# Optimization experiments

Hardware: AMD Instinct MI355X
Metric: run time of the kernel (lower is better)

Reference implementation:

```python
import jax, jax.numpy as jnp
import numpy as np

B, T = 32, 50
CONCEPT_NUM = 500
C = CONCEPT_NUM + 1          # self.concept_num = concept_num + 1
H, E = 32, 32                # hidden_dim, embedding_dim
BN_SCALE = 1.0 / np.sqrt(1.0 + 1e-5)  # eval-mode BatchNorm1d, default running stats


def _mlp(x, w1, b1, w2, b2):
    # MLP: relu(fc1) -> (dropout off in eval) -> relu(fc2) -> BatchNorm1d(eval)
    x = jax.nn.relu(x @ w1.T + b1)
    x = jax.nn.relu(x @ w2.T + b2)
    return x * BN_SCALE


def _gru(x, h, w_ih, w_hh, b_ih, b_hh):
    # torch.nn.GRUCell semantics; gate order r, z, n
    gx = x @ w_ih.T + b_ih
    gh = h @ w_hh.T + b_hh
    hd = h.shape[-1]
    r = jax.nn.sigmoid(gx[..., :hd] + gh[..., :hd])
    z = jax.nn.sigmoid(gx[..., hd:2 * hd] + gh[..., hd:2 * hd])
    n = jnp.tanh(gx[..., 2 * hd:] + r * gh[..., 2 * hd:])
    return (1.0 - z) * n + z * h


def setup_inputs() -> dict:
    key = jax.random.key(0)
    ks = jax.random.split(key, 32)
    HE = H + E
    def lin(k, out_d, in_d):
        return jax.random.normal(k, (out_d, in_d), jnp.float32) * (1.0 / np.sqrt(in_d))
    inp = {
        'features': jax.random.randint(ks[0], (B, T), 0, 2 * C, jnp.int64),
        'questions': jax.random.randint(ks[1], (B, T), 0, C, jnp.int64),
        'graph': jax.random.uniform(ks[2], (C, C), jnp.float32),
        'emb_x': jax.random.normal(ks[3], (2 * C, E), jnp.float32),
        'emb_c': jax.random.normal(ks[4], (C, E), jnp.float32),
        # f_self: MLP(H+E -> H -> H)
        'self_w1': lin(ks[5], H, HE), 'self_b1': jnp.full((H,), 0.1, jnp.float32),
        'self_w2': lin(ks[6], H, H),  'self_b2': jnp.full((H,), 0.1, jnp.float32),
        # f_neighbor_list[0]: MLP(2*(H+E) -> H -> H)
        'n0_w1': lin(ks[7], H, 2 * HE), 'n0_b1': jnp.full((H,), 0.1, jnp.float32),
        'n0_w2': lin(ks[8], H, H),      'n0_b2': jnp.full((H,), 0.1, jnp.float32),
        # f_neighbor_list[1]
        'n1_w1': lin(ks[9], H, 2 * HE),  'n1_b1': jnp.full((H,), 0.1, jnp.float32),
        'n1_w2': lin(ks[10], H, H),      'n1_b2': jnp.full((H,), 0.1, jnp.float32),
        # EraseAddGate
        'ea_w': jax.random.uniform(ks[11], (C,), jnp.float32, -1.0, 1.0) / np.sqrt(C),
        'ea_ew': lin(ks[12], H, H), 'ea_eb': jnp.zeros((H,), jnp.float32),
        'ea_aw': lin(ks[13], H, H), 'ea_ab': jnp.zeros((H,), jnp.float32),
        # GRUCell
        'gru_w_ih': lin(ks[14], 3 * H, H), 'gru_w_hh': lin(ks[15], 3 * H, H),
        'gru_b_ih': jnp.zeros((3 * H,), jnp.float32), 'gru_b_hh': jnp.zeros((3 * H,), jnp.float32),
        # predict
        'pred_w': lin(ks[16], 1, H), 'pred_b': jnp.zeros((1,), jnp.float32),
    }
    return inp


def reference(features, questions, graph, emb_x, emb_c,
              self_w1, self_b1, self_w2, self_b2,
              n0_w1, n0_b1, n0_w2, n0_b2,
              n1_w1, n1_b1, n1_w2, n1_b2,
              ea_w, ea_ew, ea_eb, ea_aw, ea_ab,
              gru_w_ih, gru_w_hh, gru_b_ih, gru_b_hh,
              pred_w, pred_b):
    b_ar = jnp.arange(B)

    def step(ht, inp):
        xt, qt = inp  # [B], [B]
        # _aggregate: response embedding via one_hot(xt) @ emb_x == gather
        res_emb = emb_x[xt]                                          # [B, E]
        ce = jnp.broadcast_to(emb_c[None], (B, C, E))                # [B, C, E]
        ce = ce.at[b_ar, qt].set(res_emb)
        tmp_ht = jnp.concatenate([ht, ce], axis=-1)                  # [B, C, H+E]
        # _agg_neighbors (Dense graph, 2 edge types)
        self_ht = tmp_ht[b_ar, qt]                                   # [B, H+E]
        self_feat = _mlp(self_ht, self_w1, self_b1, self_w2, self_b2)
        neigh_ht = jnp.concatenate(
            [jnp.broadcast_to(self_ht[:, None], tmp_ht.shape), tmp_ht], axis=-1)  # [B, C, 2(H+E)]
        adj = graph[qt][..., None]                                   # [B, C, 1]
        radj = graph[:, qt].T[..., None]                             # [B, C, 1]
        neigh = adj * _mlp(neigh_ht, n0_w1, n0_b1, n0_w2, n0_b2) \
              + radj * _mlp(neigh_ht, n1_w1, n1_b1, n1_w2, n1_b2)    # [B, C, H]
        m = neigh.at[b_ar, qt].set(self_feat)
        # EraseAddGate
        eg = jax.nn.sigmoid(m @ ea_ew.T + ea_eb)
        af = jnp.tanh(m @ ea_aw.T + ea_ab)
        w = ea_w[None, :, None]
        m = m - w * eg * m + w * af
        # GRUCell over every (student, concept)
        h_next = _gru(m.reshape(-1, H), ht.reshape(-1, H),
                      gru_w_ih, gru_w_hh, gru_b_ih, gru_b_hh).reshape(B, C, H)
        yt = jax.nn.sigmoid((h_next @ pred_w.T + pred_b)[..., 0])    # [B, C]
        return h_next, yt

    ht0 = jnp.zeros((B, C, H), dtype=graph.dtype)
    _, yts = jax.lax.scan(step, ht0, (features.T, questions.T))      # [T, B, C]
    # _get_next_pred: prediction for question at t+1 from state after step t
    yts = jnp.moveaxis(yts[:-1], 0, 1)                               # [B, T-1, C]
    q_next = questions[:, 1:]                                        # [B, T-1]
    pred = jnp.take_along_axis(yts, q_next[..., None], axis=-1)[..., 0]
    return pred                                                      # [B, T-1]
```

## Files before the change

### kernel.cpp

```cpp
#include <hip/hip_runtime.h>
#include <math.h>

#define BB 32
#define TT 50
#define CC 501
#define NNODES (BB*CC)
#define GPB 32
#define NTHREADS (GPB*32)
#define NBLK (NNODES/GPB)
#define BN_SCALEF 0.9999950000374996f

#define HT_SZ   (NNODES*32)
#define P_SZ    (CC*32)
#define GT_SZ   (CC*CC)
#define PERB_BUF (BB*96)

__device__ __forceinline__ float dot4(float4 a, float4 b){
    return a.x*b.x + a.y*b.y + a.z*b.z + a.w*b.w;
}
__device__ __forceinline__ float sigm(float x){ return 1.f/(1.f+__expf(-x)); }
__device__ __forceinline__ float tanhfast(float x){ return 1.f - 2.f/(__expf(2.f*x)+1.f); }

__global__ void init0_kernel(const float* __restrict__ graph,
                             float* __restrict__ graphT,
                             float* __restrict__ ht) {
    int i = blockIdx.x*blockDim.x + threadIdx.x;
    if (i < HT_SZ) ht[i] = 0.f;
    if (i < GT_SZ) {
        int r = i / CC, c2 = i % CC;
        graphT[i] = graph[c2*CC + r];
    }
}

__global__ void pk_kernel(const float* __restrict__ n0_w1, const float* __restrict__ n1_w1,
                          const float* __restrict__ emb_c,
                          float* __restrict__ P0, float* __restrict__ P1) {
    int c = blockIdx.x;
    int which = threadIdx.x >> 5, j = threadIdx.x & 31;
    float ec = emb_c[c*32 + j];
    const float* W = which ? n1_w1 : n0_w1;
    float acc = 0.f;
    #pragma unroll
    for (int k = 0; k < 32; k++)
        acc += W[j*128 + 96 + k] * __shfl(ec, k, 32);
    (which ? P1 : P0)[c*32 + j] = acc;
}

__global__ void perb0_kernel(const int* __restrict__ features, const float* __restrict__ emb_x,
                             const float* __restrict__ n0_w1, const float* __restrict__ n0_b1,
                             const float* __restrict__ n1_w1, const float* __restrict__ n1_b1,
                             const float* __restrict__ self_w1, const float* __restrict__ self_b1,
                             const float* __restrict__ self_w2, const float* __restrict__ self_b2,
                             float* __restrict__ perb) {
    int b = threadIdx.x >> 5, j = threadIdx.x & 31;
    int xt = features[b*TT + 0];
    float eq = emb_x[xt*32 + j];
    float a0 = n0_b1[j], a1 = n1_b1[j], s = self_b1[j];
    #pragma unroll
    for (int k = 0; k < 32; k++) {
        float ek = __shfl(eq, k, 32);
        a0 += n0_w1[j*128 + 32 + k] * ek;
        a1 += n1_w1[j*128 + 32 + k] * ek;
        s  += self_w1[j*64 + 32 + k] * ek;
    }
    float l1 = fmaxf(s, 0.f);
    float s2 = self_b2[j];
    #pragma unroll
    for (int k = 0; k < 32; k++) s2 += self_w2[j*32 + k] * __shfl(l1, k, 32);
    perb[b*96 + j]      = a0;
    perb[b*96 + 32 + j] = a1;
    perb[b*96 + 64 + j] = fmaxf(s2, 0.f) * BN_SCALEF;
}

__global__ __launch_bounds__(NTHREADS) void step_kernel(
    int t,
    const int* __restrict__ features, const int* __restrict__ questions,
    const float* __restrict__ graph,  const float* __restrict__ emb_x,
    const float* __restrict__ self_w1, const float* __restrict__ self_b1,
    const float* __restrict__ self_w2, const float* __restrict__ self_b2,
    const float* __restrict__ n0_w1, const float* __restrict__ n0_b1,
    const float* __restrict__ n0_w2, const float* __restrict__ n0_b2,
    const float* __restrict__ n1_w1, const float* __restrict__ n1_b1,
    const float* __restrict__ n1_w2, const float* __restrict__ n1_b2,
    const float* __restrict__ ea_w,  const float* __restrict__ ea_ew,
    const float* __restrict__ ea_eb, const float* __restrict__ ea_aw,
    const float* __restrict__ ea_ab,
    const float* __restrict__ gru_w_ih, const float* __restrict__ gru_w_hh,
    const float* __restrict__ gru_b_ih, const float* __restrict__ gru_b_hh,
    const float* __restrict__ pred_w,   const float* __restrict__ pred_b,
    float* __restrict__ ht,
    const float* __restrict__ P0, const float* __restrict__ P1,
    const float* __restrict__ graphT,
    float* __restrict__ perb, float* __restrict__ out)
{
    __shared__ float Wq[12288];
    __shared__ float bufH[GPB][36];
    __shared__ float bufA[GPB][36];
    __shared__ float bufB[GPB][36];

    int tid = threadIdx.x;
    for (int idx = tid; idx < 12288; idx += NTHREADS) {
        float v;
        if (idx < 6144) {
            int region = idx >> 10;
            int r = idx & 1023;
            int j = (r >> 2) & 31;
            int k = ((r >> 7) << 2) | (r & 3);
            switch (region) {
                case 0:  v = n0_w1[j*128 + 64 + k]; break;
                case 1:  v = n1_w1[j*128 + 64 + k]; break;
                case 2:  v = n0_w2[j*32 + k]; break;
                case 3:  v = n1_w2[j*32 + k]; break;
                case 4:  v = ea_ew[j*32 + k]; break;
                default: v = ea_aw[j*32 + k]; break;
            }
            Wq[idx] = v;
        } else {
            int r = idx - 6144;
            int which = r / 3072;
            int r2 = r % 3072;
            int row = (r2 >> 2) % 96;
            int k = ((r2 / 384) << 2) | (r2 & 3);
            Wq[idx] = which ? gru_w_hh[row*32 + k] : gru_w_ih[row*32 + k];
        }
    }

    int g = tid >> 5, j = tid & 31;
    int node = blockIdx.x * GPB + g;
    int b = node / CC, c = node % CC;
    int qt = questions[b*TT + t];
    float adj  = graph [qt*CC + c];
    float radj = graphT[qt*CC + c];
    float h_j = ht[node*32 + j];
    bufH[g][j] = h_j;
    __syncthreads();

    const float* pb = perb + (t & 1) * PERB_BUF + b*96;

    float acc0 = pb[j]      + P0[c*32 + j];
    float acc1 = pb[32 + j] + P1[c*32 + j];
    {
        const float4* xh = (const float4*)bufH[g];
        #pragma unroll
        for (int kc = 0; kc < 8; kc++) {
            float4 x  = xh[kc];
            float4 w0 = *(const float4*)&Wq[       kc*128 + j*4];
            float4 w1 = *(const float4*)&Wq[1024 + kc*128 + j*4];
            acc0 += dot4(w0, x);
            acc1 += dot4(w1, x);
        }
    }
    bufA[g][j] = fmaxf(acc0, 0.f);
    bufB[g][j] = fmaxf(acc1, 0.f);

    float a0 = n0_b2[j], a1 = n1_b2[j];
    {
        const float4* xa = (const float4*)bufA[g];
        const float4* xb = (const float4*)bufB[g];
        #pragma unroll
        for (int kc = 0; kc < 8; kc++) {
            float4 va = xa[kc], vb = xb[kc];
            float4 w0 = *(const float4*)&Wq[2048 + kc*128 + j*4];
            float4 w1 = *(const float4*)&Wq[3072 + kc*128 + j*4];
            a0 += dot4(w0, va);
            a1 += dot4(w1, vb);
        }
    }
    float f0 = fmaxf(a0, 0.f) * BN_SCALEF;
    float f1 = fmaxf(a1, 0.f) * BN_SCALEF;
    float m = adj*f0 + radj*f1;
    if (c == qt) m = pb[64 + j];
    bufA[g][j] = m;

    float e = ea_eb[j], aa = ea_ab[j];
    {
        const float4* xm = (const float4*)bufA[g];
        #pragma unroll
        for (int kc = 0; kc < 8; kc++) {
            float4 vm = xm[kc];
            float4 we = *(const float4*)&Wq[4096 + kc*128 + j*4];
            float4 wa = *(const float4*)&Wq[5120 + kc*128 + j*4];
            e  += dot4(we, vm);
            aa += dot4(wa, vm);
        }
    }
    float eg = sigm(e);
    float af = tanhfast(aa);
    float wc = ea_w[c];
    float mm = m - wc*eg*m + wc*af;
    bufB[g][j] = mm;

    float g0 = gru_b_ih[j], g1 = gru_b_ih[32+j], g2 = gru_b_ih[64+j];
    float hh0 = gru_b_hh[j], hh1 = gru_b_hh[32+j], hh2 = gru_b_hh[64+j];
    {
        const float4* xm = (const float4*)bufB[g];
        const float4* xh = (const float4*)bufH[g];
        #pragma unroll
        for (int kc = 0; kc < 8; kc++) {
            float4 vm = xm[kc], vh = xh[kc];
            const float* wi = &Wq[6144 + kc*384];
            const float* wh = &Wq[9216 + kc*384];
            float4 wi0 = *(const float4*)&wi[j*4];
            float4 wi1 = *(const float4*)&wi[(32+j)*4];
            float4 wi2 = *(const float4*)&wi[(64+j)*4];
            float4 wh0 = *(const float4*)&wh[j*4];
            float4 wh1 = *(const float4*)&wh[(32+j)*4];
            float4 wh2 = *(const float4*)&wh[(64+j)*4];
            g0  += dot4(wi0, vm);  g1  += dot4(wi1, vm);  g2  += dot4(wi2, vm);
            hh0 += dot4(wh0, vh);  hh1 += dot4(wh1, vh);  hh2 += dot4(wh2, vh);
        }
    }
    float r = sigm(g0 + hh0);
    float z = sigm(g1 + hh1);
    float n = tanhfast(g2 + r*hh2);
    float hn = (1.f - z)*n + z*h_j;
    ht[node*32 + j] = hn;

    int qn = questions[b*TT + t + 1];
    if (c == qn) {
        float v = hn * pred_w[j];
        #pragma unroll
        for (int off = 16; off; off >>= 1) v += __shfl_down(v, off, 32);
        if (j == 0) out[b*(TT-1) + t] = sigm(v + pred_b[0]);

        if (t < TT - 2) {
            int xt1 = features[b*TT + t + 1];
            float eq = emb_x[xt1*32 + j];
            float accA0 = n0_b1[j], accA1 = n1_b1[j], accS = self_b1[j];
            #pragma unroll
            for (int k = 0; k < 32; k++) {
                float hk = __shfl(hn, k, 32);
                float ek = __shfl(eq, k, 32);
                accA0 += n0_w1[j*128 + k]*hk + n0_w1[j*128 + 32 + k]*ek;
                accA1 += n1_w1[j*128 + k]*hk + n1_w1[j*128 + 32 + k]*ek;
                accS  += self_w1[j*64 + k]*hk + self_w1[j*64 + 32 + k]*ek;
            }
            float l1 = fmaxf(accS, 0.f);
            float s2 = self_b2[j];
            #pragma unroll
            for (int k = 0; k < 32; k++) s2 += self_w2[j*32 + k] * __shfl(l1, k, 32);
            float* pn = perb + ((t+1) & 1) * PERB_BUF + b*96;
            pn[j]      = accA0;
            pn[32 + j] = accA1;
            pn[64 + j] = fmaxf(s2, 0.f) * BN_SCALEF;
        }
    }
}

extern "C" void kernel_launch(void* const* d_in, const int* in_sizes, int n_in,
                              void* d_out, int out_size, void* d_ws, size_t ws_size,
                              hipStream_t stream) {
    const int*   features = (const int*)  d_in[0];
    const int*   questions= (const int*)  d_in[1];
    const float* graph    = (const float*)d_in[2];
    const float* emb_x    = (const float*)d_in[3];
    const float* emb_c    = (const float*)d_in[4];
    const float* self_w1  = (const float*)d_in[5];
    const float* self_b1  = (const float*)d_in[6];
    const float* self_w2  = (const float*)d_in[7];
    const float* self_b2  = (const float*)d_in[8];
    const float* n0_w1    = (const float*)d_in[9];
    const float* n0_b1    = (const float*)d_in[10];
    const float* n0_w2    = (const float*)d_in[11];
    const float* n0_b2    = (const float*)d_in[12];
    const float* n1_w1    = (const float*)d_in[13];
    const float* n1_b1    = (const float*)d_in[14];
    const float* n1_w2    = (const float*)d_in[15];
    const float* n1_b2    = (const float*)d_in[16];
    const float* ea_w     = (const float*)d_in[17];
    const float* ea_ew    = (const float*)d_in[18];
    const float* ea_eb    = (const float*)d_in[19];
    const float* ea_aw    = (const float*)d_in[20];
    const float* ea_ab    = (const float*)d_in[21];
    const float* gru_w_ih = (const float*)d_in[22];
    const float* gru_w_hh = (const float*)d_in[23];
    const float* gru_b_ih = (const float*)d_in[24];
    const float* gru_b_hh = (const float*)d_in[25];
    const float* pred_w   = (const float*)d_in[26];
    const float* pred_b   = (const float*)d_in[27];
    float* out = (float*)d_out;

    float* ws     = (float*)d_ws;
    float* ht     = ws;
    float* P0     = ht + HT_SZ;
    float* P1     = P0 + P_SZ;
    float* graphT = P1 + P_SZ;
    float* perb   = graphT + GT_SZ;

    init0_kernel<<<(HT_SZ + 255)/256, 256, 0, stream>>>(graph, graphT, ht);
    pk_kernel<<<CC, 64, 0, stream>>>(n0_w1, n1_w1, emb_c, P0, P1);
    perb0_kernel<<<1, NTHREADS, 0, stream>>>(features, emb_x,
        n0_w1, n0_b1, n1_w1, n1_b1, self_w1, self_b1, self_w2, self_b2, perb);

    for (int t = 0; t < TT - 1; t++) {
        step_kernel<<<NBLK, NTHREADS, 0, stream>>>(
            t, features, questions, graph, emb_x,
            self_w1, self_b1, self_w2, self_b2,
            n0_w1, n0_b1, n0_w2, n0_b2,
            n1_w1, n1_b1, n1_w2, n1_b2,
            ea_w, ea_ew, ea_eb, ea_aw, ea_ab,
            gru_w_ih, gru_w_hh, gru_b_ih, gru_b_hh,
            pred_w, pred_b,
            ht, P0, P1, graphT, perb, out);
    }
}
```

Before: 1.017 ms.

## Process multiple nodes per thread to reuse shared-memory weight loads

Each 64-lane wave now handles 8 nodes, with every thread accumulating 4 nodes at once, so each float4 weight read from shared memory serves several nodes. Blocks shrink to 512 threads covering 64 nodes, which cuts the per-block weight-staging overhead relative to useful work and lowers the shared-memory weight traffic per FLOP. The cost is more registers per thread, which may reduce occupancy, and fewer, larger blocks.

New measurement: 1.128 ms. 1.11x slower.

```diff
diff --git a/kernel.cpp b/kernel.cpp
--- a/kernel.cpp
+++ b/kernel.cpp
@@ -5,10 +5,14 @@
 #define TT 50
 #define CC 501
 #define NNODES (BB*CC)
-#define GPB 32
-#define NTHREADS (GPB*32)
-#define NBLK (NNODES/GPB)
 #define BN_SCALEF 0.9999950000374996f
+
+#define V 4
+#define NPW 8
+#define WPB 8
+#define NTH 512
+#define NPB (NPW*WPB)
+#define NBLK ((NNODES + NPB - 1)/NPB)
 
 #define HT_SZ   (NNODES*32)
 #define P_SZ    (CC*32)
@@ -72,7 +76,7 @@
     perb[b*96 + 64 + j] = fmaxf(s2, 0.f) * BN_SCALEF;
 }
 
-__global__ __launch_bounds__(NTHREADS) void step_kernel(
+__global__ __launch_bounds__(NTH) void step_kernel(
     int t,
     const int* __restrict__ features, const int* __restrict__ questions,
     const float* __restrict__ graph,  const float* __restrict__ emb_x,
@@ -94,12 +98,10 @@
     float* __restrict__ perb, float* __restrict__ out)
 {
     __shared__ float Wq[12288];
-    __shared__ float bufH[GPB][36];
-    __shared__ float bufA[GPB][36];
-    __shared__ float bufB[GPB][36];
+    __shared__ float xb[WPB][3][NPW][32];
 
     int tid = threadIdx.x;
-    for (int idx = tid; idx < 12288; idx += NTHREADS) {
+    for (int idx = tid; idx < 12288; idx += NTH) {
         float v;
         if (idx < 6144) {
             int region = idx >> 10;
@@ -125,124 +127,186 @@
         }
     }
 
-    int g = tid >> 5, j = tid & 31;
-    int node = blockIdx.x * GPB + g;
-    int b = node / CC, c = node % CC;
-    int qt = questions[b*TT + t];
-    float adj  = graph [qt*CC + c];
-    float radj = graphT[qt*CC + c];
-    float h_j = ht[node*32 + j];
-    bufH[g][j] = h_j;
+    int l   = tid & 63;
+    int w   = tid >> 6;
+    int j   = l & 31, sub = l >> 5;
+    int nodebase = blockIdx.x*NPB + w*NPW;
+    bool act = nodebase < NNODES;
+
+    int nodev[V], bv[V], cv[V], qtv[V], pbo[V];
+    float hj[V], adjv[V], radjv[V];
+    if (act) {
+        #pragma unroll
+        for (int v = 0; v < V; v++) {
+            int node = nodebase + 2*v + sub;
+            nodev[v] = node;
+            int b = node / CC;
+            int c = node - b*CC;
+            bv[v] = b; cv[v] = c;
+            int qt = questions[b*TT + t];
+            qtv[v] = qt;
+            adjv[v]  = graph [qt*CC + c];
+            radjv[v] = graphT[qt*CC + c];
+            pbo[v] = (t & 1)*PERB_BUF + b*96;
+            float h = ht[node*32 + j];
+            hj[v] = h;
+            xb[w][0][2*v+sub][j] = h;
+        }
+    }
     __syncthreads();
-
-    const float* pb = perb + (t & 1) * PERB_BUF + b*96;
-
-    float acc0 = pb[j]      + P0[c*32 + j];
-    float acc1 = pb[32 + j] + P1[c*32 + j];
+    if (!act) return;
+
+    float acc0[V], acc1[V];
+    #pragma unroll
+    for (int v = 0; v < V; v++) {
+        acc0[v] = perb[pbo[v] + j]      + P0[cv[v]*32 + j];
+        acc1[v] = perb[pbo[v] + 32 + j] + P1[cv[v]*32 + j];
+    }
+    #pragma unroll
+    for (int kc = 0; kc < 8; kc++) {
+        float4 w0 = *(const float4*)&Wq[       kc*128 + j*4];
+        float4 w1 = *(const float4*)&Wq[1024 + kc*128 + j*4];
+        #pragma unroll
+        for (int v = 0; v < V; v++) {
+            float4 x = *(const float4*)&xb[w][0][2*v+sub][kc*4];
+            acc0[v] += dot4(w0, x);
+            acc1[v] += dot4(w1, x);
+        }
+    }
+    #pragma unroll
+    for (int v = 0; v < V; v++) {
+        xb[w][1][2*v+sub][j] = fmaxf(acc0[v], 0.f);
+        xb[w][2][2*v+sub][j] = fmaxf(acc1[v], 0.f);
+    }
+
+    float a0[V], a1[V];
     {
-        const float4* xh = (const float4*)bufH[g];
-        #pragma unroll
-        for (int kc = 0; kc < 8; kc++) {
-            float4 x  = xh[kc];
-            float4 w0 = *(const float4*)&Wq[       kc*128 + j*4];
-            float4 w1 = *(const float4*)&Wq[1024 + kc*128 + j*4];
-            acc0 += dot4(w0, x);
-            acc1 += dot4(w1, x);
-        }
-    }
-    bufA[g][j] = fmaxf(acc0, 0.f);
-    bufB[g][j] = fmaxf(acc1, 0.f);
-
-    float a0 = n0_b2[j], a1 = n1_b2[j];
+        float b0 = n0_b2[j], b1 = n1_b2[j];
+        #pragma unroll
+        for (int v = 0; v < V; v++) { a0[v] = b0; a1[v] = b1; }
+    }
+    #pragma unroll
+    for (int kc = 0; kc < 8; kc++) {
+        float4 w0 = *(const float4*)&Wq[2048 + kc*128 + j*4];
+        float4 w1 = *(const float4*)&Wq[3072 + kc*128 + j*4];
+        #pragma unroll
+        for (int v = 0; v < V; v++) {
+            float4 va = *(const float4*)&xb[w][1][2*v+sub][kc*4];
+            float4 vb = *(const float4*)&xb[w][2][2*v+sub][kc*4];
+            a0[v] += dot4(w0, va);
+            a1[v] += dot4(w1, vb);
+        }
+    }
+    float mval[V];
+    #pragma unroll
+    for (int v = 0; v < V; v++) {
+        float f0 = fmaxf(a0[v], 0.f) * BN_SCALEF;
+        float f1 = fmaxf(a1[v], 0.f) * BN_SCALEF;
+        float m = adjv[v]*f0 + radjv[v]*f1;
+        if (cv[v] == qtv[v]) m = perb[pbo[v] + 64 + j];
+        mval[v] = m;
+    }
+    #pragma unroll
+    for (int v = 0; v < V; v++) xb[w][1][2*v+sub][j] = mval[v];
+
+    float e[V], aa[V];
     {
-        const float4* xa = (const float4*)bufA[g];
-        const float4* xb = (const float4*)bufB[g];
-        #pragma unroll
-        for (int kc = 0; kc < 8; kc++) {
-            float4 va = xa[kc], vb = xb[kc];
-            float4 w0 = *(const float4*)&Wq[2048 + kc*128 + j*4];
-            float4 w1 = *(const float4*)&Wq[3072 + kc*128 + j*4];
-            a0 += dot4(w0, va);
-            a1 += dot4(w1, vb);
-        }
-    }
-    float f0 = fmaxf(a0, 0.f) * BN_SCALEF;
-    float f1 = fmaxf(a1, 0.f) * BN_SCALEF;
-    float m = adj*f0 + radj*f1;
-    if (c == qt) m = pb[64 + j];
-    bufA[g][j] = m;
-
-    float e = ea_eb[j], aa = ea_ab[j];
+        float be = ea_eb[j], ba = ea_ab[j];
+        #pragma unroll
+        for (int v = 0; v < V; v++) { e[v] = be; aa[v] = ba; }
+    }
+    #pragma unroll
+    for (int kc = 0; kc < 8; kc++) {
+        float4 we = *(const float4*)&Wq[4096 + kc*128 + j*4];
+        float4 wa = *(const float4*)&Wq[5120 + kc*128 + j*4];
+        #pragma unroll
+        for (int v = 0; v < V; v++) {
+            float4 vm = *(const float4*)&xb[w][1][2*v+sub][kc*4];
+            e[v]  += dot4(we, vm);
+            aa[v] += dot4(wa, vm);
+        }
+    }
+    #pragma unroll
+    for (int v = 0; v < V; v++) {
+        float eg = sigm(e[v]);
+        float af = tanhfast(aa[v]);
+        float wc = ea_w[cv[v]];
+        float m  = mval[v];
+        xb[w][2][2*v+sub][j] = m - wc*eg*m + wc*af;
+    }
+
+    float gi0[V], gi1[V], gi2[V], gh0[V], gh1[V], gh2[V];
     {
-        const float4* xm = (const float4*)bufA[g];
-        #pragma unroll
-        for (int kc = 0; kc < 8; kc++) {
-            float4 vm = xm[kc];
-            float4 we = *(const float4*)&Wq[4096 + kc*128 + j*4];
-            float4 wa = *(const float4*)&Wq[5120 + kc*128 + j*4];
-            e  += dot4(we, vm);
-            aa += dot4(wa, vm);
-        }
-    }
-    float eg = sigm(e);
-    float af = tanhfast(aa);
-    float wc = ea_w[c];
-    float mm = m - wc*eg*m + wc*af;
-    bufB[g][j] = mm;
-
-    float g0 = gru_b_ih[j], g1 = gru_b_ih[32+j], g2 = gru_b_ih[64+j];
-    float hh0 = gru_b_hh[j], hh1 = gru_b_hh[32+j], hh2 = gru_b_hh[64+j];
-    {
-        const float4* xm = (const float4*)bufB[g];
-        const float4* xh = (const float4*)bufH[g];
-        #pragma unroll
-        for (int kc = 0; kc < 8; kc++) {
-            float4 vm = xm[kc], vh = xh[kc];
-            const float* wi = &Wq[6144 + kc*384];
-            const float* wh = &Wq[9216 + kc*384];
-            float4 wi0 = *(const float4*)&wi[j*4];
-            float4 wi1 = *(const float4*)&wi[(32+j)*4];
-            float4 wi2 = *(const float4*)&wi[(64+j)*4];
-            float4 wh0 = *(const float4*)&wh[j*4];
-            float4 wh1 = *(const float4*)&wh[(32+j)*4];
-            float4 wh2 = *(const float4*)&wh[(64+j)*4];
-            g0  += dot4(wi0, vm);  g1  += dot4(wi1, vm);  g2  += dot4(wi2, vm);
-            hh0 += dot4(wh0, vh);  hh1 += dot4(wh1, vh);  hh2 += dot4(wh2, vh);
-        }
-    }
-    float r = sigm(g0 + hh0);
-    float z = sigm(g1 + hh1);
-    float n = tanhfast(g2 + r*hh2);
-    float hn = (1.f - z)*n + z*h_j;
-    ht[node*32 + j] = hn;
-
-    int qn = questions[b*TT + t + 1];
-    if (c == qn) {
-        float v = hn * pred_w[j];
-        #pragma unroll
-        for (int off = 16; off; off >>= 1) v += __shfl_down(v, off, 32);
-        if (j == 0) out[b*(TT-1) + t] = sigm(v + pred_b[0]);
-
-        if (t < TT - 2) {
-            int xt1 = features[b*TT + t + 1];
-            float eq = emb_x[xt1*32 + j];
-            float accA0 = n0_b1[j], accA1 = n1_b1[j], accS = self_b1[j];
+        float bi0 = gru_b_ih[j], bi1 = gru_b_ih[32+j], bi2 = gru_b_ih[64+j];
+        float bh0 = gru_b_hh[j], bh1 = gru_b_hh[32+j], bh2 = gru_b_hh[64+j];
+        #pragma unroll
+        for (int v = 0; v < V; v++) {
+            gi0[v]=bi0; gi1[v]=bi1; gi2[v]=bi2;
+            gh0[v]=bh0; gh1[v]=bh1; gh2[v]=bh2;
+        }
+    }
+    #pragma unroll
+    for (int kc = 0; kc < 8; kc++) {
+        const float* wi = &Wq[6144 + kc*384];
+        const float* wh = &Wq[9216 + kc*384];
+        float4 wi0 = *(const float4*)&wi[j*4];
+        float4 wi1 = *(const float4*)&wi[(32+j)*4];
+        float4 wi2 = *(const float4*)&wi[(64+j)*4];
+        float4 wh0 = *(const float4*)&wh[j*4];
+        float4 wh1 = *(const float4*)&wh[(32+j)*4];
+        float4 wh2 = *(const float4*)&wh[(64+j)*4];
+        #pragma unroll
+        for (int v = 0; v < V; v++) {
+            float4 vm = *(const float4*)&xb[w][2][2*v+sub][kc*4];
+            float4 vh = *(const float4*)&xb[w][0][2*v+sub][kc*4];
+            gi0[v] += dot4(wi0, vm);
+            gi1[v] += dot4(wi1, vm);
+            gi2[v] += dot4(wi2, vm);
+            gh0[v] += dot4(wh0, vh);
+            gh1[v] += dot4(wh1, vh);
+            gh2[v] += dot4(wh2, vh);
+        }
+    }
+    float hn[V];
+    #pragma unroll
+    for (int v = 0; v < V; v++) {
+        float r = sigm(gi0[v] + gh0[v]);
+        float z = sigm(gi1[v] + gh1[v]);
+        float n = tanhfast(gi2[v] + r*gh2[v]);
+        hn[v] = (1.f - z)*n + z*hj[v];
+        ht[nodev[v]*32 + j] = hn[v];
+    }
+
+    #pragma unroll
+    for (int v = 0; v < V; v++) {
+        int qn = questions[bv[v]*TT + t + 1];
+        if (cv[v] == qn) {
+            float s = hn[v] * pred_w[j];
             #pragma unroll
-            for (int k = 0; k < 32; k++) {
-                float hk = __shfl(hn, k, 32);
-                float ek = __shfl(eq, k, 32);
-                accA0 += n0_w1[j*128 + k]*hk + n0_w1[j*128 + 32 + k]*ek;
-                accA1 += n1_w1[j*128 + k]*hk + n1_w1[j*128 + 32 + k]*ek;
-                accS  += self_w1[j*64 + k]*hk + self_w1[j*64 + 32 + k]*ek;
+            for (int off = 16; off; off >>= 1) s += __shfl_down(s, off, 32);
+            if (j == 0) out[bv[v]*(TT-1) + t] = sigm(s + pred_b[0]);
+
+            if (t < TT - 2) {
+                int xt1 = features[bv[v]*TT + t + 1];
+                float eq = emb_x[xt1*32 + j];
+                float accA0 = n0_b1[j], accA1 = n1_b1[j], accS = self_b1[j];
+                #pragma unroll
+                for (int k = 0; k < 32; k++) {
+                    float hk = __shfl(hn[v], k, 32);
+                    float ek = __shfl(eq, k, 32);
+                    accA0 += n0_w1[j*128 + k]*hk + n0_w1[j*128 + 32 + k]*ek;
+                    accA1 += n1_w1[j*128 + k]*hk + n1_w1[j*128 + 32 + k]*ek;
+                    accS  += self_w1[j*64 + k]*hk + self_w1[j*64 + 32 + k]*ek;
+                }
+                float l1 = fmaxf(accS, 0.f);
+                float s2 = self_b2[j];
+                #pragma unroll
+                for (int k = 0; k < 32; k++) s2 += self_w2[j*32 + k] * __shfl(l1, k, 32);
+                float* pn = perb + ((t+1) & 1)*PERB_BUF + bv[v]*96;
+                pn[j]      = accA0;
+                pn[32 + j] = accA1;
+                pn[64 + j] = fmaxf(s2, 0.f) * BN_SCALEF;
             }
-            float l1 = fmaxf(accS, 0.f);
-            float s2 = self_b2[j];
-            #pragma unroll
-            for (int k = 0; k < 32; k++) s2 += self_w2[j*32 + k] * __shfl(l1, k, 32);
-            float* pn = perb + ((t+1) & 1) * PERB_BUF + b*96;
-            pn[j]      = accA0;
-            pn[32 + j] = accA1;
-            pn[64 + j] = fmaxf(s2, 0.f) * BN_SCALEF;
         }
     }
 }
@@ -289,11 +353,11 @@
 
     init0_kernel<<<(HT_SZ + 255)/256, 256, 0, stream>>>(graph, graphT, ht);
     pk_kernel<<<CC, 64, 0, stream>>>(n0_w1, n1_w1, emb_c, P0, P1);
-    perb0_kernel<<<1, NTHREADS, 0, stream>>>(features, emb_x,
+    perb0_kernel<<<1, 1024, 0, stream>>>(features, emb_x,
         n0_w1, n0_b1, n1_w1, n1_b1, self_w1, self_b1, self_w2, self_b2, perb);
 
     for (int t = 0; t < TT - 1; t++) {
-        step_kernel<<<NBLK, NTHREADS, 0, stream>>>(
+        step_kernel<<<NBLK, NTH, 0, stream>>>(
             t, features, questions, graph, emb_x,
             self_w1, self_b1, self_w2, self_b2,
             n0_w1, n0_b1, n0_w2, n0_b2,
```
